# Performance work log

Measured on AMD Instinct MI355X. Metric: run time of the kernel, lower is better.

Reference implementation:

```python
import jax, jax.numpy as jnp
import numpy as np

B, T, O, D, H, EA, R, NB = 64, 90, 5, 256, 256, 4096, 5, 8
NPG = T + O          # nodes per graph
N = B * NPG          # total nodes


def setup_inputs() -> dict:
    key = jax.random.key(0)
    ks = jax.random.split(key, 11)
    M = jax.random.normal(ks[0], (B, T, D), jnp.float32)            # r_out proxy
    x = jax.random.normal(ks[1], (N, D), jnp.float32)               # graph_input nodes
    node_att = jax.random.uniform(ks[2], (B, T, O), jnp.float32)    # softmax(f_predicts) proxy
    edge_src = jax.random.randint(ks[3], (B, EA), 0, T, jnp.int32)
    edge_dst = jax.random.randint(ks[4], (B, EA), 0, T, jnp.int32)
    edge_type = jax.random.randint(ks[5], (B, EA), 0, R, jnp.int32)
    Ws = jax.random.normal(ks[6], (T, D), jnp.float32) / np.float32(np.sqrt(D))       # EdgeAttention.scalar (max_seq_len x D)
    bases = jax.random.normal(ks[7], (NB, D, H), jnp.float32) / np.float32(np.sqrt(D))  # RGCN basis weights
    comp = jax.random.normal(ks[8], (R, NB), jnp.float32) / np.float32(np.sqrt(NB))
    root = jax.random.normal(ks[9], (D, H), jnp.float32) / np.float32(np.sqrt(D))
    bias = jnp.zeros((H,), jnp.float32)
    return dict(M=M, x=x, node_att=node_att, Ws=Ws, bases=bases, comp=comp,
                root=root, bias=bias, edge_src=edge_src, edge_dst=edge_dst,
                edge_type=edge_type)


def reference(M, x, node_att, Ws, bases, comp, root, bias, edge_src, edge_dst, edge_type):
    # ---- EdgeAttention: scale = Linear(M)[:, :, :T]; softmax over dim=1; permute(0,2,1) ----
    scale = jnp.einsum('btd,sd->bts', M, Ws)[:, :, :T]        # [B,T,T]
    alpha = jax.nn.softmax(scale, axis=1).transpose(0, 2, 1)  # [B,T,T]

    # ---- edge_norm gather: scores[b, src, dst] for attention edges, node_att for tag edges ----
    b_idx = jnp.arange(B)[:, None]
    norm_att = alpha[b_idx, edge_src, edge_dst]               # [B,EA]
    norm_tag = node_att.reshape(B, T * O)                     # node_att[b].view(-1)
    edge_norm = jnp.concatenate([norm_att, norm_tag], axis=1).reshape(-1)  # [E]

    # ---- build block-diagonal batched edge index (tag edges: utt i -> user node T+o) ----
    tag_src = jnp.broadcast_to(jnp.repeat(jnp.arange(T, dtype=jnp.int32), O), (B, T * O))
    tag_dst = jnp.broadcast_to(T + jnp.tile(jnp.arange(O, dtype=jnp.int32), T), (B, T * O))
    src_l = jnp.concatenate([edge_src, tag_src], axis=1)
    dst_l = jnp.concatenate([edge_dst, tag_dst], axis=1)
    et = jnp.concatenate([edge_type, jnp.full((B, T * O), R - 1, jnp.int32)], axis=1)
    offset = (jnp.arange(B, dtype=jnp.int32) * NPG)[:, None]
    src = (src_l + offset).reshape(-1)                        # [E] global src
    dst = (dst_l + offset).reshape(-1)                        # [E] global dst
    et = et.reshape(-1)                                       # [E]

    # ---- basis-decomposed RGCN: msg_e = edge_norm_e * (x[src_e] @ W[type_e]) ----
    W = jnp.einsum('rn,ndh->rdh', comp, bases)                # [R,D,H]
    x_e = x[src]                                              # [E,D] irregular gather
    msg = jnp.zeros((src.shape[0], H), x.dtype)
    for r in range(R):                                        # loop over few relations (structural)
        msg = msg + jnp.where((et == r)[:, None], x_e @ W[r], jnp.zeros((), x.dtype))
    msg = msg * edge_norm[:, None]
    agg = jax.ops.segment_sum(msg, dst, num_segments=N)       # scatter-add at dst
    out = agg + x @ root + bias                               # self/root transform + bias
    return out.reshape(B, NPG, H)                             # graph_out.view(B, T+O, -1)
```

## Files before the change

### kernel.cpp

```cpp
#include <hip/hip_runtime.h>
#include <cstddef>
#include <cstdint>

#define Bq 64
#define Tq 90
#define Oq 5
#define Dq 256
#define Hq 256
#define EAq 4096
#define Rq 5
#define NBq 8
#define NPGq 95
#define Nq 6080
#define NPq 6144
#define EPBq 4546
#define Eq 290944
#define KAq 480

typedef __attribute__((ext_vector_type(8))) short bf16x8;
typedef __attribute__((ext_vector_type(8))) unsigned short u16x8;
typedef __attribute__((ext_vector_type(4))) float f32x4;
typedef __attribute__((address_space(1))) const unsigned int gu32;
typedef __attribute__((address_space(3))) unsigned int lu32;

__device__ __forceinline__ unsigned short f2bf(float f) {
    unsigned u = __float_as_uint(f);
    unsigned r = (u + 0x7FFF + ((u >> 16) & 1)) >> 16;
    return (unsigned short)r;
}
__device__ __forceinline__ float bf2f(unsigned short s) {
    return __uint_as_float(((unsigned)s) << 16);
}

__global__ __launch_bounds__(576) void k_pa(const float* __restrict__ M,
                                            const float* __restrict__ Ws,
                                            const float* __restrict__ natt,
                                            const int* __restrict__ esrc,
                                            const int* __restrict__ edst,
                                            const int* __restrict__ etype,
                                            const float* __restrict__ x,
                                            const float* __restrict__ bases,
                                            const float* __restrict__ comp,
                                            const float* __restrict__ rootw,
                                            unsigned short* __restrict__ A2b,
                                            unsigned short* __restrict__ xb,
                                            unsigned short* __restrict__ Wt) {
    __shared__ __attribute__((aligned(16))) char lds[99072];
    const int tid = threadIdx.x;
    const int w = tid >> 6, l = tid & 63;
    const int blk = blockIdx.x;

    if (blk >= 64 && blk < 406) {
        unsigned i = (unsigned)(blk - 64) * 576 + tid;
        if (i < NPq * 32) {
            unsigned np = i >> 5, c = i & 31;
            unsigned s = np % 96;
            u16x8 pk;
            if (s == 95) {
#pragma unroll
                for (int q = 0; q < 8; ++q) pk[q] = 0;
            } else {
                unsigned node = np - np / 96;
                const float4* xs = (const float4*)(x + (size_t)node * Dq + c * 8);
                float4 a = xs[0], b2 = xs[1];
                pk[0] = f2bf(a.x);  pk[1] = f2bf(a.y);  pk[2] = f2bf(a.z);  pk[3] = f2bf(a.w);
                pk[4] = f2bf(b2.x); pk[5] = f2bf(b2.y); pk[6] = f2bf(b2.z); pk[7] = f2bf(b2.w);
            }
            *(u16x8*)(xb + (size_t)np * Dq + c * 8) = pk;
        }
        return;
    }
    if (blk >= 406) {
        float* Ld = (float*)lds;
        int wblk = blk - 406;
        int rs = wblk >> 3;
        int d0 = (wblk & 7) * 32;
        int t = tid;
        if (t < 256) {
            float cmp[NBq];
            if (rs < Rq)
#pragma unroll
                for (int nb = 0; nb < NBq; ++nb) cmp[nb] = comp[rs * NBq + nb];
            for (int dl = 0; dl < 32; ++dl) {
                int d = d0 + dl;
                float v;
                if (rs < Rq) {
                    v = 0.f;
#pragma unroll
                    for (int nb = 0; nb < NBq; ++nb)
                        v += cmp[nb] * bases[((size_t)nb * Dq + d) * Hq + t];
                } else {
                    v = rootw[(size_t)d * Hq + t];
                }
                Ld[dl * 257 + t] = v;
            }
        }
        __syncthreads();
        if (t < 256) {
            int c = t & 31, hg = t >> 5;
            for (int hh = 0; hh < 32; ++hh) {
                int h = hg * 32 + hh;
                Wt[(size_t)(rs * 256 + h) * Dq + d0 + c] = f2bf(Ld[c * 257 + h]);
            }
        }
        return;
    }

    unsigned short* Mb = (unsigned short*)lds;
    unsigned short* Wb = (unsigned short*)(lds + 49152);
    float* P   = (float*)lds;
    float* Acc = (float*)(lds + 49152);
    float* mxs = (float*)(lds + 98304);
    float* rds = (float*)(lds + 98688);
    const int b = blk;

    int es[8], ed[8], et[8];
#pragma unroll
    for (int k = 0; k < 8; ++k) {
        int j = tid + k * 576;
        if (j < EAq) {
            es[k] = esrc[(size_t)b * EAq + j];
            ed[k] = edst[(size_t)b * EAq + j];
            et[k] = etype[(size_t)b * EAq + j];
        }
    }
    float tagv = (tid < Tq * Oq) ? natt[(size_t)b * (Tq * Oq) + tid] : 0.f;

#pragma unroll
    for (int i = 0; i < 6; ++i) {
        int idx = tid + i * 576;
        if (idx < 3072) {
            int row = idx >> 5, c = idx & 31;
            u16x8 pm, pw;
            if (row < Tq) {
                const float4* ms = (const float4*)(M + ((size_t)b * Tq + row) * Dq + c * 8);
                float4 a0 = ms[0], a1 = ms[1];
                pm[0] = f2bf(a0.x); pm[1] = f2bf(a0.y); pm[2] = f2bf(a0.z); pm[3] = f2bf(a0.w);
                pm[4] = f2bf(a1.x); pm[5] = f2bf(a1.y); pm[6] = f2bf(a1.z); pm[7] = f2bf(a1.w);
                const float4* ws = (const float4*)(Ws + (size_t)row * Dq + c * 8);
                float4 w0 = ws[0], w1 = ws[1];
                pw[0] = f2bf(w0.x); pw[1] = f2bf(w0.y); pw[2] = f2bf(w0.z); pw[3] = f2bf(w0.w);
                pw[4] = f2bf(w1.x); pw[5] = f2bf(w1.y); pw[6] = f2bf(w1.z); pw[7] = f2bf(w1.w);
            } else {
#pragma unroll
                for (int q = 0; q < 8; ++q) { pm[q] = 0; pw[q] = 0; }
            }
            int off = row * 512 + ((c * 16) ^ ((row & 7) << 4));
            *(u16x8*)((char*)Mb + off) = pm;
            *(u16x8*)((char*)Wb + off) = pw;
        }
    }
    __syncthreads();

    const int wr = w / 3, wc = w % 3;
    f32x4 acc[2][2];
#pragma unroll
    for (int i = 0; i < 2; ++i)
#pragma unroll
        for (int j = 0; j < 2; ++j) acc[i][j] = (f32x4)0.0f;
#pragma unroll
    for (int ks = 0; ks < 8; ++ks) {
        int kb = ks * 64 + (l >> 4) * 16;
        bf16x8 af[2], bfv[2];
#pragma unroll
        for (int mi = 0; mi < 2; ++mi) {
            int row = wr * 32 + mi * 16 + (l & 15);
            af[mi] = *(const bf16x8*)((char*)Mb + row * 512 + (kb ^ ((row & 7) << 4)));
        }
#pragma unroll
        for (int ni = 0; ni < 2; ++ni) {
            int row = wc * 32 + ni * 16 + (l & 15);
            bfv[ni] = *(const bf16x8*)((char*)Wb + row * 512 + (kb ^ ((row & 7) << 4)));
        }
#pragma unroll
        for (int mi = 0; mi < 2; ++mi)
#pragma unroll
            for (int ni = 0; ni < 2; ++ni)
                acc[mi][ni] = __builtin_amdgcn_mfma_f32_16x16x32_bf16(
                    af[mi], bfv[ni], acc[mi][ni], 0, 0, 0);
    }
    __syncthreads();

#pragma unroll
    for (int mi = 0; mi < 2; ++mi)
#pragma unroll
        for (int ni = 0; ni < 2; ++ni)
#pragma unroll
            for (int j = 0; j < 4; ++j) {
                int rowp = wr * 32 + mi * 16 + (l >> 4) * 4 + j;
                int colp = wc * 32 + ni * 16 + (l & 15);
                P[rowp * 97 + colp] = acc[mi][ni][j];
            }
    __syncthreads();

    if (tid < 96) {
        float m = -1e30f;
        for (int t = 0; t < Tq; ++t) m = fmaxf(m, P[t * 97 + tid]);
        float s = 0.f;
        for (int t = 0; t < Tq; ++t) s += __expf(P[t * 97 + tid] - m);
        mxs[tid] = m;
        rds[tid] = 1.f / s;
    }
    __syncthreads();

    float v[8];
#pragma unroll
    for (int k = 0; k < 8; ++k) {
        int j = tid + k * 576;
        if (j < EAq)
            v[k] = __expf(P[ed[k] * 97 + es[k]] - mxs[es[k]]) * rds[es[k]];
    }

    for (int r = 0; r < Rq; ++r) {
#pragma unroll
        for (int i = 0; i < 4; ++i)
            ((float4*)Acc)[tid + i * 576] = make_float4(0.f, 0.f, 0.f, 0.f);
        __syncthreads();
#pragma unroll
        for (int k = 0; k < 8; ++k) {
            int j = tid + k * 576;
            if (j < EAq && et[k] == r)
                atomicAdd(&Acc[ed[k] * 96 + es[k]], v[k]);
        }
        if (r == Rq - 1 && tid < Tq * Oq) {
            int t = tid / Oq, o = tid % Oq;
            Acc[(Tq + o) * 96 + t] = tagv;
        }
        __syncthreads();
#pragma unroll
        for (int i = 0; i < 2; ++i) {
            int c0 = tid + i * 576;
            const float* src = Acc + (c0 / 12) * 96 + (c0 % 12) * 8;
            u16x8 pk;
#pragma unroll
            for (int q = 0; q < 8; ++q) pk[q] = f2bf(src[q]);
            *(u16x8*)(A2b + ((size_t)b * 96 + c0 / 12) * KAq + r * 96 + (c0 % 12) * 8) = pk;
        }
        __syncthreads();
    }
}

__global__ __launch_bounds__(512) void k_gemm3(const unsigned short* __restrict__ A2b,
                                               const unsigned short* __restrict__ Wt,
                                               const unsigned short* __restrict__ xb,
                                               const float* __restrict__ bias,
                                               float* __restrict__ out) {
    __shared__ __attribute__((aligned(16))) char lds[145408];
    char* const Xs  = lds;
    char* const Wl0 = lds + 49152;
    char* const Wl1 = lds + 81920;
    char* const Ztl = lds + 114688;
    char* const A2l = lds + 126976;
    const int hc = blockIdx.x;
    const int b  = blockIdx.y;
    const int tid = threadIdx.x;
    const int w = tid >> 6, l = tid & 63;
    const int wrz = w >> 1, wcz = w & 1;
    const int wrn = w >> 2, wcn = w & 3;

#pragma unroll
    for (int i = 0; i < 6; ++i) {
        int idx = i * 512 + tid;
        int row = idx >> 5, c = idx & 31;
        const unsigned short* g = xb + (size_t)(b * 96 + row) * Dq + (c ^ (row & 7)) * 8;
        __builtin_amdgcn_global_load_lds((gu32*)g,
            (lu32*)(unsigned int)(uintptr_t)(Xs + idx * 16), 16, 0, 0);
    }

    f32x4 acc[3];
#pragma unroll
    for (int i = 0; i < 3; ++i) acc[i] = (f32x4)0.0f;

    auto stageW = [&](char* Wbuf, int slice) {
        int kkbase = slice * 256 + hc * 64;
#pragma unroll
        for (int i = 0; i < 4; ++i) {
            int idx = i * 512 + tid;
            int hrow = idx >> 5, c = idx & 31;
            const unsigned short* g = Wt + (size_t)(kkbase + hrow) * Dq + (c ^ (hrow & 7)) * 8;
            __builtin_amdgcn_global_load_lds((gu32*)g,
                (lu32*)(unsigned int)(uintptr_t)(Wbuf + idx * 16), 16, 0, 0);
        }
    };
    auto stageA2 = [&](int r) {
#pragma unroll
        for (int i = 0; i < 3; ++i) {
            int idx = i * 512 + tid;
            if (idx < 1152) {
                int row = idx / 12, u = idx - row * 12;
                int usw = u ^ (row & 3);
                const unsigned short* g = A2b + ((size_t)b * 96 + row) * KAq + r * 96 + usw * 8;
                __builtin_amdgcn_global_load_lds((gu32*)g,
                    (lu32*)(unsigned int)(uintptr_t)(A2l + idx * 16), 16, 0, 0);
            }
        }
    };
    auto gemmZ = [&](char* Wbuf, f32x4 (&zacc)[3]) {
#pragma unroll
        for (int i = 0; i < 3; ++i) zacc[i] = (f32x4)0.0f;
#pragma unroll
        for (int ks = 0; ks < 8; ++ks) {
            int kb = ks * 64 + (l >> 4) * 16;
            int hl = wrz * 16 + (l & 15);
            bf16x8 af = *(const bf16x8*)(Wbuf + hl * 512 + (kb ^ ((hl & 7) << 4)));
#pragma unroll
            for (int ni = 0; ni < 3; ++ni) {
                int s = wcz * 48 + ni * 16 + (l & 15);
                bf16x8 xv = *(const bf16x8*)(Xs + s * 512 + (kb ^ ((s & 7) << 4)));
                zacc[ni] = __builtin_amdgcn_mfma_f32_16x16x32_bf16(af, xv, zacc[ni], 0, 0, 0);
            }
        }
    };
    auto writeZt = [&](f32x4 (&zacc)[3]) {
#pragma unroll
        for (int ni = 0; ni < 3; ++ni)
#pragma unroll
            for (int j = 0; j < 4; ++j) {
                int h = wrz * 16 + (l >> 4) * 4 + j;
                int s = wcz * 48 + ni * 16 + (l & 15);
                *(unsigned short*)(Ztl + h * 192 + (((s >> 3) ^ (h & 3)) << 4) + (s & 7) * 2)
                    = f2bf(zacc[ni][j]);
            }
    };

    stageW(Wl0, 0);
    stageA2(0);
    __syncthreads();

    char* Wcur = Wl0;
    char* Wnxt = Wl1;
    for (int r = 0; r < Rq; ++r) {
        f32x4 zacc[3];
        gemmZ(Wcur, zacc);
        stageW(Wnxt, r + 1);
        writeZt(zacc);
        __syncthreads();
#pragma unroll
        for (int ks = 0; ks < 3; ++ks) {
            int kb = ks * 64 + (l >> 4) * 16;
            int h = wcn * 16 + (l & 15);
            bf16x8 bfv = *(const bf16x8*)(Ztl + h * 192 + (kb ^ ((h & 3) << 4)));
#pragma unroll
            for (int mi = 0; mi < 3; ++mi) {
                int nl = wrn * 48 + mi * 16 + (l & 15);
                bf16x8 af = *(const bf16x8*)(A2l + nl * 192 + (kb ^ ((nl & 3) << 4)));
                acc[mi] = __builtin_amdgcn_mfma_f32_16x16x32_bf16(af, bfv, acc[mi], 0, 0, 0);
            }
        }
        __syncthreads();
        if (r < Rq - 1) stageA2(r + 1);
        char* t2 = Wcur; Wcur = Wnxt; Wnxt = t2;
    }

    f32x4 zacc[3];
    gemmZ(Wcur, zacc);
    writeZt(zacc);
    __syncthreads();
#pragma unroll
    for (int mi = 0; mi < 3; ++mi) {
        int h = wcn * 16 + (l & 15);
#pragma unroll
        for (int j = 0; j < 4; ++j) {
            int nl = wrn * 48 + mi * 16 + (l >> 4) * 4 + j;
            float rv = bf2f(*(const unsigned short*)(Ztl + h * 192 +
                            (((nl >> 3) ^ (h & 3)) << 4) + (nl & 7) * 2));
            acc[mi][j] += rv;
        }
    }

    {
        int h = wcn * 16 + (l & 15);
        float bv = bias[hc * 64 + h];
#pragma unroll
        for (int mi = 0; mi < 3; ++mi)
#pragma unroll
            for (int j = 0; j < 4; ++j) {
                int nl = wrn * 48 + mi * 16 + (l >> 4) * 4 + j;
                if (nl < NPGq)
                    out[((size_t)b * NPGq + nl) * Hq + hc * 64 + h] = acc[mi][j] + bv;
            }
    }
}

extern "C" void kernel_launch(void* const* d_in, const int* in_sizes, int n_in,
                              void* d_out, int out_size, void* d_ws, size_t ws_size,
                              hipStream_t stream) {
    (void)in_sizes; (void)n_in; (void)out_size; (void)ws_size;
    const float* M     = (const float*)d_in[0];
    const float* x     = (const float*)d_in[1];
    const float* natt  = (const float*)d_in[2];
    const float* Ws    = (const float*)d_in[3];
    const float* bases = (const float*)d_in[4];
    const float* comp  = (const float*)d_in[5];
    const float* rootw = (const float*)d_in[6];
    const float* bias  = (const float*)d_in[7];
    const int* esrc    = (const int*)d_in[8];
    const int* edst    = (const int*)d_in[9];
    const int* etype   = (const int*)d_in[10];
    float* out = (float*)d_out;
    char* ws = (char*)d_ws;

    unsigned short* Wt  = (unsigned short*)(ws + 0);
    unsigned short* A2b = (unsigned short*)(ws + 786432);
    unsigned short* xb  = (unsigned short*)(ws + 6684672);

    k_pa<<<dim3(454), 576, 0, stream>>>(M, Ws, natt, esrc, edst, etype,
                                        x, bases, comp, rootw, A2b, xb, Wt);
    k_gemm3<<<dim3(4, Bq), 512, 0, stream>>>(A2b, Wt, xb, bias, out);
}
```

Measured before the change: 41.14 us.

## Fuse attention softmax, adjacency build and RGCN GEMM into one per-batch kernel

Splits weight combination into a small standalone kernel and merges the attention/adjacency stage with the per-relation GEMM into one kernel, so each block builds its dense relation adjacency and bf16 x tile directly in LDS instead of round-tripping A2b and xb through global memory. This removes intermediate global writes and reads and one kernel boundary. In exchange, each of the 4 H-chunk blocks per graph recomputes the M·Ws attention GEMM and softmax, the W tile is single-buffered with extra barriers, and one of nine waves sits idle during the GEMM phases.

```diff
diff --git a/kernel.cpp b/kernel.cpp
--- a/kernel.cpp
+++ b/kernel.cpp
@@ -11,11 +11,6 @@
 #define Rq 5
 #define NBq 8
 #define NPGq 95
-#define Nq 6080
-#define NPq 6144
-#define EPBq 4546
-#define Eq 290944
-#define KAq 480
 
 typedef __attribute__((ext_vector_type(8))) short bf16x8;
 typedef __attribute__((ext_vector_type(8))) unsigned short u16x8;
@@ -32,87 +27,66 @@
     return __uint_as_float(((unsigned)s) << 16);
 }
 
-__global__ __launch_bounds__(576) void k_pa(const float* __restrict__ M,
-                                            const float* __restrict__ Ws,
-                                            const float* __restrict__ natt,
-                                            const int* __restrict__ esrc,
-                                            const int* __restrict__ edst,
-                                            const int* __restrict__ etype,
-                                            const float* __restrict__ x,
-                                            const float* __restrict__ bases,
+__global__ __launch_bounds__(256) void k_wt(const float* __restrict__ bases,
                                             const float* __restrict__ comp,
                                             const float* __restrict__ rootw,
-                                            unsigned short* __restrict__ A2b,
-                                            unsigned short* __restrict__ xb,
                                             unsigned short* __restrict__ Wt) {
-    __shared__ __attribute__((aligned(16))) char lds[99072];
-    const int tid = threadIdx.x;
-    const int w = tid >> 6, l = tid & 63;
-    const int blk = blockIdx.x;
-
-    if (blk >= 64 && blk < 406) {
-        unsigned i = (unsigned)(blk - 64) * 576 + tid;
-        if (i < NPq * 32) {
-            unsigned np = i >> 5, c = i & 31;
-            unsigned s = np % 96;
-            u16x8 pk;
-            if (s == 95) {
-#pragma unroll
-                for (int q = 0; q < 8; ++q) pk[q] = 0;
-            } else {
-                unsigned node = np - np / 96;
-                const float4* xs = (const float4*)(x + (size_t)node * Dq + c * 8);
-                float4 a = xs[0], b2 = xs[1];
-                pk[0] = f2bf(a.x);  pk[1] = f2bf(a.y);  pk[2] = f2bf(a.z);  pk[3] = f2bf(a.w);
-                pk[4] = f2bf(b2.x); pk[5] = f2bf(b2.y); pk[6] = f2bf(b2.z); pk[7] = f2bf(b2.w);
-            }
-            *(u16x8*)(xb + (size_t)np * Dq + c * 8) = pk;
-        }
-        return;
-    }
-    if (blk >= 406) {
-        float* Ld = (float*)lds;
-        int wblk = blk - 406;
-        int rs = wblk >> 3;
-        int d0 = (wblk & 7) * 32;
-        int t = tid;
-        if (t < 256) {
-            float cmp[NBq];
-            if (rs < Rq)
-#pragma unroll
-                for (int nb = 0; nb < NBq; ++nb) cmp[nb] = comp[rs * NBq + nb];
-            for (int dl = 0; dl < 32; ++dl) {
-                int d = d0 + dl;
-                float v;
-                if (rs < Rq) {
-                    v = 0.f;
-#pragma unroll
-                    for (int nb = 0; nb < NBq; ++nb)
-                        v += cmp[nb] * bases[((size_t)nb * Dq + d) * Hq + t];
-                } else {
-                    v = rootw[(size_t)d * Hq + t];
-                }
-                Ld[dl * 257 + t] = v;
-            }
-        }
-        __syncthreads();
-        if (t < 256) {
-            int c = t & 31, hg = t >> 5;
-            for (int hh = 0; hh < 32; ++hh) {
-                int h = hg * 32 + hh;
-                Wt[(size_t)(rs * 256 + h) * Dq + d0 + c] = f2bf(Ld[c * 257 + h]);
-            }
-        }
-        return;
-    }
-
+    __shared__ float Ld[32][257];
+    int wblk = blockIdx.x;
+    int rs = wblk >> 3;
+    int d0 = (wblk & 7) * 32;
+    int t = threadIdx.x;
+    float cmp[NBq];
+    if (rs < Rq)
+#pragma unroll
+        for (int nb = 0; nb < NBq; ++nb) cmp[nb] = comp[rs * NBq + nb];
+    for (int dl = 0; dl < 32; ++dl) {
+        int d = d0 + dl;
+        float v;
+        if (rs < Rq) {
+            v = 0.f;
+#pragma unroll
+            for (int nb = 0; nb < NBq; ++nb)
+                v += cmp[nb] * bases[((size_t)nb * Dq + d) * Hq + t];
+        } else {
+            v = rootw[(size_t)d * Hq + t];
+        }
+        Ld[dl][t] = v;
+    }
+    __syncthreads();
+    int c = t & 31, hg = t >> 5;
+    for (int hh = 0; hh < 32; ++hh) {
+        int h = hg * 32 + hh;
+        Wt[(size_t)(rs * 256 + h) * Dq + d0 + c] = f2bf(Ld[c][h]);
+    }
+}
+
+__global__ __launch_bounds__(576) void k_fused(const float* __restrict__ M,
+                                               const float* __restrict__ Ws,
+                                               const float* __restrict__ natt,
+                                               const int* __restrict__ esrc,
+                                               const int* __restrict__ edst,
+                                               const int* __restrict__ etype,
+                                               const float* __restrict__ x,
+                                               const unsigned short* __restrict__ Wt,
+                                               const float* __restrict__ bias,
+                                               float* __restrict__ out) {
+    __shared__ __attribute__((aligned(16))) char lds[137984];
     unsigned short* Mb = (unsigned short*)lds;
     unsigned short* Wb = (unsigned short*)(lds + 49152);
     float* P   = (float*)lds;
-    float* Acc = (float*)(lds + 49152);
-    float* mxs = (float*)(lds + 98304);
-    float* rds = (float*)(lds + 98688);
-    const int b = blk;
+    float* mxs = (float*)(lds + 137216);
+    float* rds = (float*)(lds + 137600);
+    char* const Xs   = lds;
+    char* const Wl   = lds + 49152;
+    float* const Acc = (float*)(lds + 81920);
+    char* const Ztl  = lds + 81920;
+    char* const A2l  = lds + 118784;
+
+    const int tid = threadIdx.x;
+    const int w = tid >> 6, l = tid & 63;
+    const int b  = blockIdx.x & 63;
+    const int hc = blockIdx.x >> 6;
 
     int es[8], ed[8], et[8];
 #pragma unroll
@@ -152,45 +126,47 @@
     }
     __syncthreads();
 
-    const int wr = w / 3, wc = w % 3;
-    f32x4 acc[2][2];
-#pragma unroll
-    for (int i = 0; i < 2; ++i)
-#pragma unroll
-        for (int j = 0; j < 2; ++j) acc[i][j] = (f32x4)0.0f;
-#pragma unroll
-    for (int ks = 0; ks < 8; ++ks) {
-        int kb = ks * 64 + (l >> 4) * 16;
-        bf16x8 af[2], bfv[2];
-#pragma unroll
-        for (int mi = 0; mi < 2; ++mi) {
-            int row = wr * 32 + mi * 16 + (l & 15);
-            af[mi] = *(const bf16x8*)((char*)Mb + row * 512 + (kb ^ ((row & 7) << 4)));
-        }
-#pragma unroll
-        for (int ni = 0; ni < 2; ++ni) {
-            int row = wc * 32 + ni * 16 + (l & 15);
-            bfv[ni] = *(const bf16x8*)((char*)Wb + row * 512 + (kb ^ ((row & 7) << 4)));
-        }
+    {
+        const int wr = w / 3, wc = w % 3;
+        f32x4 pacc[2][2];
+#pragma unroll
+        for (int i = 0; i < 2; ++i)
+#pragma unroll
+            for (int j = 0; j < 2; ++j) pacc[i][j] = (f32x4)0.0f;
+#pragma unroll
+        for (int ks = 0; ks < 8; ++ks) {
+            int kb = ks * 64 + (l >> 4) * 16;
+            bf16x8 af[2], bfv[2];
+#pragma unroll
+            for (int mi = 0; mi < 2; ++mi) {
+                int row = wr * 32 + mi * 16 + (l & 15);
+                af[mi] = *(const bf16x8*)((char*)Mb + row * 512 + (kb ^ ((row & 7) << 4)));
+            }
+#pragma unroll
+            for (int ni = 0; ni < 2; ++ni) {
+                int row = wc * 32 + ni * 16 + (l & 15);
+                bfv[ni] = *(const bf16x8*)((char*)Wb + row * 512 + (kb ^ ((row & 7) << 4)));
+            }
+#pragma unroll
+            for (int mi = 0; mi < 2; ++mi)
+#pragma unroll
+                for (int ni = 0; ni < 2; ++ni)
+                    pacc[mi][ni] = __builtin_amdgcn_mfma_f32_16x16x32_bf16(
+                        af[mi], bfv[ni], pacc[mi][ni], 0, 0, 0);
+        }
+        __syncthreads();
+
 #pragma unroll
         for (int mi = 0; mi < 2; ++mi)
 #pragma unroll
             for (int ni = 0; ni < 2; ++ni)
-                acc[mi][ni] = __builtin_amdgcn_mfma_f32_16x16x32_bf16(
-                    af[mi], bfv[ni], acc[mi][ni], 0, 0, 0);
-    }
-    __syncthreads();
-
-#pragma unroll
-    for (int mi = 0; mi < 2; ++mi)
-#pragma unroll
-        for (int ni = 0; ni < 2; ++ni)
-#pragma unroll
-            for (int j = 0; j < 4; ++j) {
-                int rowp = wr * 32 + mi * 16 + (l >> 4) * 4 + j;
-                int colp = wc * 32 + ni * 16 + (l & 15);
-                P[rowp * 97 + colp] = acc[mi][ni][j];
-            }
+#pragma unroll
+                for (int j = 0; j < 4; ++j) {
+                    int rowp = wr * 32 + mi * 16 + (l >> 4) * 4 + j;
+                    int colp = wc * 32 + ni * 16 + (l & 15);
+                    P[rowp * 97 + colp] = pacc[mi][ni][j];
+                }
+    }
     __syncthreads();
 
     if (tid < 96) {
@@ -210,99 +186,50 @@
         if (j < EAq)
             v[k] = __expf(P[ed[k] * 97 + es[k]] - mxs[es[k]]) * rds[es[k]];
     }
-
-    for (int r = 0; r < Rq; ++r) {
-#pragma unroll
-        for (int i = 0; i < 4; ++i)
-            ((float4*)Acc)[tid + i * 576] = make_float4(0.f, 0.f, 0.f, 0.f);
-        __syncthreads();
-#pragma unroll
-        for (int k = 0; k < 8; ++k) {
-            int j = tid + k * 576;
-            if (j < EAq && et[k] == r)
-                atomicAdd(&Acc[ed[k] * 96 + es[k]], v[k]);
-        }
-        if (r == Rq - 1 && tid < Tq * Oq) {
-            int t = tid / Oq, o = tid % Oq;
-            Acc[(Tq + o) * 96 + t] = tagv;
-        }
-        __syncthreads();
-#pragma unroll
-        for (int i = 0; i < 2; ++i) {
-            int c0 = tid + i * 576;
-            const float* src = Acc + (c0 / 12) * 96 + (c0 % 12) * 8;
+    __syncthreads();
+
+#pragma unroll
+    for (int i = 0; i < 6; ++i) {
+        int idx = tid + i * 576;
+        if (idx < 3072) {
+            int row = idx >> 5, c = idx & 31;
             u16x8 pk;
-#pragma unroll
-            for (int q = 0; q < 8; ++q) pk[q] = f2bf(src[q]);
-            *(u16x8*)(A2b + ((size_t)b * 96 + c0 / 12) * KAq + r * 96 + (c0 % 12) * 8) = pk;
-        }
-        __syncthreads();
-    }
-}
-
-__global__ __launch_bounds__(512) void k_gemm3(const unsigned short* __restrict__ A2b,
-                                               const unsigned short* __restrict__ Wt,
-                                               const unsigned short* __restrict__ xb,
-                                               const float* __restrict__ bias,
-                                               float* __restrict__ out) {
-    __shared__ __attribute__((aligned(16))) char lds[145408];
-    char* const Xs  = lds;
-    char* const Wl0 = lds + 49152;
-    char* const Wl1 = lds + 81920;
-    char* const Ztl = lds + 114688;
-    char* const A2l = lds + 126976;
-    const int hc = blockIdx.x;
-    const int b  = blockIdx.y;
-    const int tid = threadIdx.x;
-    const int w = tid >> 6, l = tid & 63;
+            if (row < NPGq) {
+                const float4* xs4 = (const float4*)(x + ((size_t)b * NPGq + row) * Dq + c * 8);
+                float4 a = xs4[0], b2 = xs4[1];
+                pk[0] = f2bf(a.x);  pk[1] = f2bf(a.y);  pk[2] = f2bf(a.z);  pk[3] = f2bf(a.w);
+                pk[4] = f2bf(b2.x); pk[5] = f2bf(b2.y); pk[6] = f2bf(b2.z); pk[7] = f2bf(b2.w);
+            } else {
+#pragma unroll
+                for (int q = 0; q < 8; ++q) pk[q] = 0;
+            }
+            *(u16x8*)(Xs + row * 512 + ((c * 16) ^ ((row & 7) << 4))) = pk;
+        }
+    }
+
+    auto stageW = [&](int slice) {
+        int kkbase = slice * 256 + hc * 64;
+#pragma unroll
+        for (int i = 0; i < 4; ++i) {
+            int idx = i * 576 + tid;
+            if (idx < 2048) {
+                int hrow = idx >> 5, c = idx & 31;
+                const unsigned short* g = Wt + (size_t)(kkbase + hrow) * Dq + (c ^ (hrow & 7)) * 8;
+                __builtin_amdgcn_global_load_lds((gu32*)g,
+                    (lu32*)(unsigned int)(uintptr_t)(Wl + idx * 16), 16, 0, 0);
+            }
+        }
+    };
     const int wrz = w >> 1, wcz = w & 1;
     const int wrn = w >> 2, wcn = w & 3;
-
-#pragma unroll
-    for (int i = 0; i < 6; ++i) {
-        int idx = i * 512 + tid;
-        int row = idx >> 5, c = idx & 31;
-        const unsigned short* g = xb + (size_t)(b * 96 + row) * Dq + (c ^ (row & 7)) * 8;
-        __builtin_amdgcn_global_load_lds((gu32*)g,
-            (lu32*)(unsigned int)(uintptr_t)(Xs + idx * 16), 16, 0, 0);
-    }
-
-    f32x4 acc[3];
-#pragma unroll
-    for (int i = 0; i < 3; ++i) acc[i] = (f32x4)0.0f;
-
-    auto stageW = [&](char* Wbuf, int slice) {
-        int kkbase = slice * 256 + hc * 64;
-#pragma unroll
-        for (int i = 0; i < 4; ++i) {
-            int idx = i * 512 + tid;
-            int hrow = idx >> 5, c = idx & 31;
-            const unsigned short* g = Wt + (size_t)(kkbase + hrow) * Dq + (c ^ (hrow & 7)) * 8;
-            __builtin_amdgcn_global_load_lds((gu32*)g,
-                (lu32*)(unsigned int)(uintptr_t)(Wbuf + idx * 16), 16, 0, 0);
-        }
-    };
-    auto stageA2 = [&](int r) {
-#pragma unroll
-        for (int i = 0; i < 3; ++i) {
-            int idx = i * 512 + tid;
-            if (idx < 1152) {
-                int row = idx / 12, u = idx - row * 12;
-                int usw = u ^ (row & 3);
-                const unsigned short* g = A2b + ((size_t)b * 96 + row) * KAq + r * 96 + usw * 8;
-                __builtin_amdgcn_global_load_lds((gu32*)g,
-                    (lu32*)(unsigned int)(uintptr_t)(A2l + idx * 16), 16, 0, 0);
-            }
-        }
-    };
-    auto gemmZ = [&](char* Wbuf, f32x4 (&zacc)[3]) {
+    auto gemmZ = [&](f32x4 (&zacc)[3]) {
 #pragma unroll
         for (int i = 0; i < 3; ++i) zacc[i] = (f32x4)0.0f;
 #pragma unroll
         for (int ks = 0; ks < 8; ++ks) {
             int kb = ks * 64 + (l >> 4) * 16;
             int hl = wrz * 16 + (l & 15);
-            bf16x8 af = *(const bf16x8*)(Wbuf + hl * 512 + (kb ^ ((hl & 7) << 4)));
+            bf16x8 af = *(const bf16x8*)(Wl + hl * 512 + (kb ^ ((hl & 7) << 4)));
 #pragma unroll
             for (int ni = 0; ni < 3; ++ni) {
                 int s = wcz * 48 + ni * 16 + (l & 15);
@@ -323,62 +250,81 @@
             }
     };
 
-    stageW(Wl0, 0);
-    stageA2(0);
-    __syncthreads();
-
-    char* Wcur = Wl0;
-    char* Wnxt = Wl1;
+    stageW(0);
+    __syncthreads();
+
+    f32x4 acc[3];
+#pragma unroll
+    for (int i = 0; i < 3; ++i) acc[i] = (f32x4)0.0f;
+
     for (int r = 0; r < Rq; ++r) {
+#pragma unroll
+        for (int i = 0; i < 4; ++i)
+            ((float4*)Acc)[tid + i * 576] = make_float4(0.f, 0.f, 0.f, 0.f);
+        __syncthreads();
+#pragma unroll
+        for (int k = 0; k < 8; ++k) {
+            int j = tid + k * 576;
+            if (j < EAq && et[k] == r)
+                atomicAdd(&Acc[ed[k] * 96 + es[k]], v[k]);
+        }
+        if (r == Rq - 1 && tid < Tq * Oq) {
+            int t = tid / Oq, o = tid % Oq;
+            Acc[(Tq + o) * 96 + t] = tagv;
+        }
+        __syncthreads();
+#pragma unroll
+        for (int i = 0; i < 2; ++i) {
+            int c0 = tid + i * 576;
+            int row = c0 / 12, u = c0 - row * 12;
+            const float* src = Acc + row * 96 + u * 8;
+            u16x8 pk;
+#pragma unroll
+            for (int q = 0; q < 8; ++q) pk[q] = f2bf(src[q]);
+            *(u16x8*)(A2l + row * 192 + ((u ^ (row & 3)) << 4)) = pk;
+        }
+        __syncthreads();
         f32x4 zacc[3];
-        gemmZ(Wcur, zacc);
-        stageW(Wnxt, r + 1);
-        writeZt(zacc);
-        __syncthreads();
-#pragma unroll
-        for (int ks = 0; ks < 3; ++ks) {
-            int kb = ks * 64 + (l >> 4) * 16;
-            int h = wcn * 16 + (l & 15);
-            bf16x8 bfv = *(const bf16x8*)(Ztl + h * 192 + (kb ^ ((h & 3) << 4)));
-#pragma unroll
-            for (int mi = 0; mi < 3; ++mi) {
-                int nl = wrn * 48 + mi * 16 + (l & 15);
-                bf16x8 af = *(const bf16x8*)(A2l + nl * 192 + (kb ^ ((nl & 3) << 4)));
-                acc[mi] = __builtin_amdgcn_mfma_f32_16x16x32_bf16(af, bfv, acc[mi], 0, 0, 0);
-            }
-        }
-        __syncthreads();
-        if (r < Rq - 1) stageA2(r + 1);
-        char* t2 = Wcur; Wcur = Wnxt; Wnxt = t2;
+        if (w < 8) gemmZ(zacc);
+        __syncthreads();
+        stageW(r + 1);
+        if (w < 8) writeZt(zacc);
+        __syncthreads();
+        if (w < 8) {
+#pragma unroll
+            for (int ks = 0; ks < 3; ++ks) {
+                int kb = ks * 64 + (l >> 4) * 16;
+                int h = wcn * 16 + (l & 15);
+                bf16x8 bfv = *(const bf16x8*)(Ztl + h * 192 + (kb ^ ((h & 3) << 4)));
+#pragma unroll
+                for (int mi = 0; mi < 3; ++mi) {
+                    int nl = wrn * 48 + mi * 16 + (l & 15);
+                    bf16x8 af = *(const bf16x8*)(A2l + nl * 192 + (kb ^ ((nl & 3) << 4)));
+                    acc[mi] = __builtin_amdgcn_mfma_f32_16x16x32_bf16(af, bfv, acc[mi], 0, 0, 0);
+                }
+            }
+        }
+        __syncthreads();
     }
 
     f32x4 zacc[3];
-    gemmZ(Wcur, zacc);
-    writeZt(zacc);
-    __syncthreads();
-#pragma unroll
-    for (int mi = 0; mi < 3; ++mi) {
-        int h = wcn * 16 + (l & 15);
-#pragma unroll
-        for (int j = 0; j < 4; ++j) {
-            int nl = wrn * 48 + mi * 16 + (l >> 4) * 4 + j;
-            float rv = bf2f(*(const unsigned short*)(Ztl + h * 192 +
-                            (((nl >> 3) ^ (h & 3)) << 4) + (nl & 7) * 2));
-            acc[mi][j] += rv;
-        }
-    }
-
-    {
+    if (w < 8) gemmZ(zacc);
+    if (w < 8) writeZt(zacc);
+    __syncthreads();
+    if (w < 8) {
         int h = wcn * 16 + (l & 15);
         float bv = bias[hc * 64 + h];
 #pragma unroll
-        for (int mi = 0; mi < 3; ++mi)
+        for (int mi = 0; mi < 3; ++mi) {
 #pragma unroll
             for (int j = 0; j < 4; ++j) {
                 int nl = wrn * 48 + mi * 16 + (l >> 4) * 4 + j;
+                float rv = bf2f(*(const unsigned short*)(Ztl + h * 192 +
+                                (((nl >> 3) ^ (h & 3)) << 4) + (nl & 7) * 2));
                 if (nl < NPGq)
-                    out[((size_t)b * NPGq + nl) * Hq + hc * 64 + h] = acc[mi][j] + bv;
-            }
+                    out[((size_t)b * NPGq + nl) * Hq + hc * 64 + h] = acc[mi][j] + rv + bv;
+            }
+        }
     }
 }
 
@@ -400,11 +346,9 @@
     float* out = (float*)d_out;
     char* ws = (char*)d_ws;
 
-    unsigned short* Wt  = (unsigned short*)(ws + 0);
-    unsigned short* A2b = (unsigned short*)(ws + 786432);
-    unsigned short* xb  = (unsigned short*)(ws + 6684672);
-
-    k_pa<<<dim3(454), 576, 0, stream>>>(M, Ws, natt, esrc, edst, etype,
-                                        x, bases, comp, rootw, A2b, xb, Wt);
-    k_gemm3<<<dim3(4, Bq), 512, 0, stream>>>(A2b, Wt, xb, bias, out);
-}
+    unsigned short* Wt = (unsigned short*)(ws + 0);
+
+    k_wt<<<dim3(48), 256, 0, stream>>>(bases, comp, rootw, Wt);
+    k_fused<<<dim3(256), 576, 0, stream>>>(M, Ws, natt, esrc, edst, etype,
+                                           x, Wt, bias, out);
+}
```

Measured after the change: 47.71 us. 1.16x slower.
